# Kernel tuning notes

Measured on AMD Instinct MI355X. Metric: run time of the kernel, lower is better.

Reference implementation:

```python
import jax, jax.numpy as jnp
import numpy as np

# --- dims ---
B_, H_IMG, W_IMG = 8, 64, 1024
C1, C2 = 32, 64
DM = 1024          # token channels = C2 * H_IMG/4
DI = 2048          # d_inner = expand * d_model
DS = 64            # d_state
DC = 4             # d_conv
NH, HD = 32, 64    # n_heads, headdim
DCONV_DIM = DI + 2 * DS           # 2176 (ngroups=1)
DPROJ = 2 * DI + 2 * DS + NH      # 4256
NB = 4             # num mamba blocks
FFH = 2 * DM       # feed-forward hidden
EPS = 1e-5


def bn(x, p, axis=1):
    # eval-mode batchnorm; p = [gamma, beta, running_mean, running_var] stacked [4, C]
    sh = [1] * x.ndim
    sh[axis] = -1
    g, b, m, v = (p[i].reshape(sh) for i in range(4))
    return (x - m) * jax.lax.rsqrt(v + EPS) * g + b


def conv2d(x, w, stride, pad):
    return jax.lax.conv_general_dilated(
        x, w, (stride, stride), [(pad, pad), (pad, pad)],
        dimension_numbers=("NCHW", "OIHW", "NCHW"))


def mamba2(u, Wi, cw, cb, dtb, A_log, Dp, nw, Wo):
    # u: [B, L, DM]  (faithful Mamba2 forward: in_proj -> causal depthwise conv
    #  + silu -> selective state scan -> gated RMSNorm -> out_proj)
    Bsz, L, _ = u.shape
    zxbcdt = jnp.einsum('bld,pd->blp', u, Wi)                  # [B,L,DPROJ]
    z, xBC, dt = jnp.split(zxbcdt, [DI, DI + DCONV_DIM], axis=-1)
    dt = jax.nn.softplus(dt + dtb)                             # [B,L,NH]
    xp = jnp.pad(xBC, ((0, 0), (DC - 1, 0), (0, 0)))           # causal pad
    xBC = sum(xp[:, k:k + L, :] * cw[:, k] for k in range(DC)) + cb
    xBC = jax.nn.silu(xBC)
    x, Bm, Cm = jnp.split(xBC, [DI, DI + DS], axis=-1)         # x:[B,L,DI] B/C:[B,L,DS]
    x = x.reshape(Bsz, L, NH, HD)
    A = -jnp.exp(A_log)                                        # [NH]
    dA = jnp.exp(dt * A)                                       # [B,L,NH]
    dtx = dt[..., None] * x                                    # [B,L,NH,HD]

    def step(h, inp):
        dA_t, dtx_t, B_t, C_t = inp
        h = h * dA_t[..., None, None] + dtx_t[..., None] * B_t[:, None, None, :]
        return h, jnp.einsum('bhpn,bn->bhp', h, C_t)

    h0 = jnp.zeros((Bsz, NH, HD, DS), u.dtype)
    _, ys = jax.lax.scan(step, h0, (dA.transpose(1, 0, 2),
                                    dtx.transpose(1, 0, 2, 3),
                                    Bm.transpose(1, 0, 2),
                                    Cm.transpose(1, 0, 2)))
    y = ys.transpose(1, 0, 2, 3) + Dp[None, None, :, None] * x  # D skip
    y = y.reshape(Bsz, L, DI)
    y = y * jax.nn.silu(z)                                      # gate
    y = y * jax.lax.rsqrt(jnp.mean(y * y, -1, keepdims=True) + EPS) * nw
    return jnp.einsum('bld,od->blo', y, Wo)                     # [B,L,DM]


def setup_inputs() -> dict:
    key = jax.random.key(0)
    ks = iter(jax.random.split(key, 80))

    def nrm(shape, s=0.02):
        return jax.random.normal(next(ks), shape, jnp.float32) * s

    def bnp(c):
        return jnp.stack([jax.random.uniform(next(ks), (c,), minval=0.5, maxval=1.5),
                          nrm((c,), 0.1), nrm((c,), 0.1),
                          jax.random.uniform(next(ks), (c,), minval=0.5, maxval=1.5)])

    inp = dict(
        image=jax.random.normal(next(ks), (B_, 1, H_IMG, W_IMG), jnp.float32),
        conv1_w=nrm((C1, 1, 7, 7), 0.1), bn1=bnp(C1),
        conv2_w=nrm((C2, C1, 7, 7), 0.05), bn2=bnp(C2),
        ds_w=nrm((C2, 1, 1, 1), 0.1), ds_bn=bnp(C2),
        in_proj_w=nrm((NB, DPROJ, DM)),
        conv1d_w=nrm((NB, DCONV_DIM, DC), 0.2), conv1d_b=nrm((NB, DCONV_DIM), 0.1),
        dt_bias=jnp.log(jnp.expm1(jax.random.uniform(next(ks), (NB, NH), minval=0.001, maxval=0.1))),
        A_log=jnp.log(jax.random.uniform(next(ks), (NB, NH), minval=1.0, maxval=16.0)),
        D=jax.random.uniform(next(ks), (NB, NH)),
        norm_w=jnp.ones((NB, DI), jnp.float32),
        out_proj_w=nrm((NB, DM, DI)),
        blk_bn=jnp.stack([bnp(DM) for _ in range(NB)]),
        ff_w1=nrm((NB, FFH, DM)), ff_b1=nrm((NB, FFH), 0.1),
        ff_bn1=jnp.stack([bnp(FFH) for _ in range(NB)]),
        ff_w2=nrm((NB, DM, FFH)), ff_b2=nrm((NB, DM), 0.1),
        ff_bn2=jnp.stack([bnp(DM) for _ in range(NB)]),
    )
    return inp


def reference(image, conv1_w, bn1, conv2_w, bn2, ds_w, ds_bn,
              in_proj_w, conv1d_w, conv1d_b, dt_bias, A_log, D, norm_w,
              out_proj_w, blk_bn, ff_w1, ff_b1, ff_bn1, ff_w2, ff_b2, ff_bn2):
    # --- conv stem with residual downsample ---
    x = bn(conv2d(image, conv1_w, 2, 3), bn1)
    x = bn(conv2d(x, conv2_w, 2, 3), bn2)
    res = bn(conv2d(image, ds_w, 4, 0), ds_bn)
    x = jax.nn.relu(x + res)                       # [B,C2,H/4,W/4]
    tokens = x.reshape(x.shape[0], -1, x.shape[3])  # image_to_sequence -> [B,DM,L]

    for i in range(NB):
        # SSMBlock: mamba2 + BN + residual
        residual = tokens
        t = mamba2(tokens.transpose(0, 2, 1), in_proj_w[i], conv1d_w[i],
                   conv1d_b[i], dt_bias[i], A_log[i], D[i], norm_w[i],
                   out_proj_w[i]).transpose(0, 2, 1)
        tokens = bn(t, blk_bn[i]) + residual
        # FeedForward (1x1 conv MLP) with residual
        residual = tokens
        h = jax.nn.relu(bn(jnp.einsum('oc,bcl->bol', ff_w1[i], tokens)
                           + ff_b1[i][:, None], ff_bn1[i]))
        tokens = bn(jnp.einsum('oc,bcl->bol', ff_w2[i], h)
                    + ff_b2[i][:, None], ff_bn2[i]) + residual
    return tokens  # [B, DM, L]
```

## Files before the change

kernel.cpp:

```cpp
#include <hip/hip_runtime.h>
#include <hip/hip_bf16.h>
#include <hip/hip_fp16.h>
#include <math.h>

#define EPSF 1e-5f
#define B_N 8
#define L_N 256
#define DM_N 1024
#define DI_N 2048
#define DS_N 64
#define NH_N 32
#define HD_N 64
#define DCONV_N 2176
#define DPROJ_N 4256
#define NTOK 2048
#define FFH_N 2048
#define NPAD_INPROJ 4352

typedef _Float16 f16x8 __attribute__((ext_vector_type(8)));
typedef float f32x4 __attribute__((ext_vector_type(4)));

__device__ __forceinline__ float sigf(float x) { return 1.f / (1.f + __expf(-x)); }

__device__ __forceinline__ void gll16(const void* g, void* l) {
  typedef __attribute__((address_space(1))) const void gv;
  typedef __attribute__((address_space(3))) void lv;
  __builtin_amdgcn_global_load_lds((gv*)g, (lv*)l, 16, 0, 0);
}

__device__ __forceinline__ f16x8 cvt8(float4 a, float4 b) {
  f16x8 o;
  o[0] = (_Float16)a.x; o[1] = (_Float16)a.y; o[2] = (_Float16)a.z; o[3] = (_Float16)a.w;
  o[4] = (_Float16)b.x; o[5] = (_Float16)b.y; o[6] = (_Float16)b.z; o[7] = (_Float16)b.w;
  return o;
}

__global__ __launch_bounds__(256) void k_tohalf8(
    const float* __restrict__ src, _Float16* __restrict__ dst, int n, int ntot) {
  int i = (blockIdx.x * 256 + threadIdx.x) * 8;
  if (i >= ntot) return;
  f16x8 o;
  if (i < n) {
    float4 a = *(const float4*)(src + i);
    float4 b = *(const float4*)(src + i + 4);
    o = cvt8(a, b);
  } else {
#pragma unroll
    for (int j = 0; j < 8; ++j) o[j] = (_Float16)0.f;
  }
  *(f16x8*)(dst + i) = o;
}

__global__ __launch_bounds__(256) void k_w1t(
    const float* __restrict__ w1, _Float16* __restrict__ W1t) {
  int i = blockIdx.x * 256 + threadIdx.x;
  if (i >= 32 * 64) return;
  int co = i >> 6, k = i & 63;
  W1t[i] = (k < 49) ? (_Float16)w1[co * 49 + k] : (_Float16)0.f;
}

__global__ __launch_bounds__(256) void k_conv1m(
    const float* __restrict__ img, const _Float16* __restrict__ W1t,
    const float* __restrict__ bnp, _Float16* __restrict__ X1h) {
  __shared__ float sIn[7][264];
  __shared__ _Float16 sA[128][72];
  __shared__ _Float16 sB[32][72];
  int b = blockIdx.x, y = blockIdx.y, x0 = blockIdx.z * 128;
  int t = threadIdx.x;
  {
    int r = t >> 3, c = (t & 7) * 8;
    *(f16x8*)&sB[r][c] = *(const f16x8*)&W1t[r * 64 + c];
  }
  const float* ip = img + (size_t)b * 64 * 1024;
#pragma unroll
  for (int r = 0; r < 7; ++r) {
    int yy = 2 * y - 3 + r;
    for (int c = t; c < 262; c += 256) {
      int xx = 2 * x0 - 3 + c;
      float v = 0.f;
      if (yy >= 0 && yy < 64 && xx >= 0 && xx < 1024) v = ip[yy * 1024 + xx];
      sIn[r][c] = v;
    }
  }
  __syncthreads();
  {
    int p = t >> 1, half = t & 1;
    _Float16 av[32];
    if (half == 0) {
#pragma unroll
      for (int k = 0; k < 32; ++k)
        av[k] = (_Float16)sIn[k / 7][2 * p + (k % 7)];
    } else {
#pragma unroll
      for (int k = 32; k < 64; ++k)
        av[k - 32] = (k < 49) ? (_Float16)sIn[k / 7][2 * p + (k % 7)] : (_Float16)0.f;
    }
    *(f16x8*)&sA[p][half * 32 + 0] = *(f16x8*)&av[0];
    *(f16x8*)&sA[p][half * 32 + 8] = *(f16x8*)&av[8];
    *(f16x8*)&sA[p][half * 32 + 16] = *(f16x8*)&av[16];
    *(f16x8*)&sA[p][half * 32 + 24] = *(f16x8*)&av[24];
  }
  __syncthreads();
  int w = t >> 6, lane = t & 63, lr = lane & 15, kh = lane >> 4;
  f32x4 acc[2][2];
#pragma unroll
  for (int i = 0; i < 2; ++i)
#pragma unroll
    for (int j = 0; j < 2; ++j) acc[i][j] = (f32x4)(0.f);
#pragma unroll
  for (int ks = 0; ks < 2; ++ks) {
    f16x8 af[2], bf[2];
#pragma unroll
    for (int i = 0; i < 2; ++i)
      af[i] = *(const f16x8*)&sA[w * 32 + i * 16 + lr][ks * 32 + kh * 8];
#pragma unroll
    for (int j = 0; j < 2; ++j)
      bf[j] = *(const f16x8*)&sB[j * 16 + lr][ks * 32 + kh * 8];
#pragma unroll
    for (int i = 0; i < 2; ++i)
#pragma unroll
      for (int j = 0; j < 2; ++j)
        acc[i][j] = __builtin_amdgcn_mfma_f32_16x16x32_f16(af[i], bf[j], acc[i][j], 0, 0, 0);
  }
#pragma unroll
  for (int j = 0; j < 2; ++j) {
    int co = j * 16 + lr;
    float g = bnp[co], be = bnp[32 + co], mm = bnp[64 + co], vv = bnp[96 + co];
    float sc = rsqrtf(vv + EPSF) * g, sh = be - mm * sc;
#pragma unroll
    for (int i = 0; i < 2; ++i) {
#pragma unroll
      for (int rr = 0; rr < 4; ++rr) {
        int pix = w * 32 + i * 16 + kh * 4 + rr;
        int x = x0 + pix;
        X1h[((size_t)(b * 32 + y) * 512 + x) * 32 + co] =
            (_Float16)fmaf(acc[i][j][rr], sc, sh);
      }
    }
  }
}

__global__ __launch_bounds__(256) void k_w2t(
    const float* __restrict__ w2, _Float16* __restrict__ W2t) {
  int i = blockIdx.x * 256 + threadIdx.x;
  if (i >= 49 * 64 * 32) return;
  int ci = i & 31, co = (i >> 5) & 63, rs = i >> 11;
  W2t[rs * 2048 + co * 32 + ci] = (_Float16)w2[co * 1568 + ci * 49 + rs];
}

__global__ __launch_bounds__(512) void k_conv2m(
    const _Float16* __restrict__ X1h, const _Float16* __restrict__ W2t,
    const float* __restrict__ bn2p, const float* __restrict__ img,
    const float* __restrict__ dsw, const float* __restrict__ dsbnp,
    _Float16* __restrict__ Tok16) {
  __shared__ _Float16 As[2][128 * 40];
  __shared__ _Float16 Bs[2][64 * 40];
  int b = blockIdx.x, ho = blockIdx.y, wo0 = blockIdx.z * 128;
  int t = threadIdx.x;
  int w = t >> 6, lane = t & 63;
  int lr = lane & 15, kh = lane >> 4;
  int wm = w >> 1, wn = w & 1;
  f32x4 acc[2][2];
#pragma unroll
  for (int i = 0; i < 2; ++i)
#pragma unroll
    for (int j = 0; j < 2; ++j) acc[i][j] = (f32x4)(0.f);

  int arow = t >> 2, achk = t & 3;
  const _Float16* xb = X1h + (size_t)b * 32 * 512 * 32;

  auto LOADA = [&](int rs, f16x8& ra) {
    int r = rs / 7, s = rs - 7 * r;
    int y = 2 * ho + r - 3;
    int xx = 2 * (wo0 + arow) + s - 3;
    if (y >= 0 && y < 32 && xx >= 0 && xx < 512)
      ra = *(const f16x8*)(xb + ((size_t)(y * 512 + xx)) * 32 + achk * 8);
    else
      ra = (f16x8)(_Float16)0.f;
  };

  f16x8 ra, rb;
  LOADA(0, ra);
  if (t < 256) rb = *(const f16x8*)(W2t + (t >> 2) * 32 + (t & 3) * 8);
  *(f16x8*)&As[0][arow * 40 + achk * 8] = ra;
  if (t < 256) *(f16x8*)&Bs[0][(t >> 2) * 40 + (t & 3) * 8] = rb;
  __syncthreads();

  int cur = 0;
  for (int rs = 0; rs < 49; ++rs) {
    f16x8 na, nb;
    if (rs + 1 < 49) {
      LOADA(rs + 1, na);
      if (t < 256)
        nb = *(const f16x8*)(W2t + (rs + 1) * 2048 + (t >> 2) * 32 + (t & 3) * 8);
    }
    f16x8 af[2], bf[2];
#pragma unroll
    for (int i = 0; i < 2; ++i)
      af[i] = *(const f16x8*)&As[cur][(wm * 32 + i * 16 + lr) * 40 + kh * 8];
#pragma unroll
    for (int j = 0; j < 2; ++j)
      bf[j] = *(const f16x8*)&Bs[cur][(wn * 32 + j * 16 + lr) * 40 + kh * 8];
#pragma unroll
    for (int i = 0; i < 2; ++i)
#pragma unroll
      for (int j = 0; j < 2; ++j)
        acc[i][j] = __builtin_amdgcn_mfma_f32_16x16x32_f16(af[i], bf[j], acc[i][j], 0, 0, 0);
    if (rs + 1 < 49) {
      *(f16x8*)&As[cur ^ 1][arow * 40 + achk * 8] = na;
      if (t < 256) *(f16x8*)&Bs[cur ^ 1][(t >> 2) * 40 + (t & 3) * 8] = nb;
      __syncthreads();
      cur ^= 1;
    }
  }

#pragma unroll
  for (int j = 0; j < 2; ++j) {
    int co = wn * 32 + j * 16 + lr;
    float g = bn2p[co], be = bn2p[64 + co], mm = bn2p[128 + co], vv = bn2p[192 + co];
    float sc = rsqrtf(vv + EPSF) * g, sh = be - mm * sc;
    float dg = dsbnp[co], dbe = dsbnp[64 + co], dmm = dsbnp[128 + co], dvv = dsbnp[192 + co];
    float dsc = rsqrtf(dvv + EPSF) * dg, dsh = dbe - dmm * dsc;
    float wv = dsw[co];
#pragma unroll
    for (int i = 0; i < 2; ++i) {
#pragma unroll
      for (int rr = 0; rr < 4; ++rr) {
        int row = wm * 32 + i * 16 + kh * 4 + rr;
        int wo = wo0 + row;
        float dval = fmaf(img[((size_t)(b * 64 + 4 * ho)) * 1024 + 4 * wo] * wv, dsc, dsh);
        float v = fmaf(acc[i][j][rr], sc, sh) + dval;
        v = v > 0.f ? v : 0.f;
        Tok16[((size_t)(b * 256 + wo)) * DM_N + co * 16 + ho] = (_Float16)v;
      }
    }
  }
}

template <int MODE, int BM, int BN>
__global__ __launch_bounds__(256) void k_mgemm(
    const _Float16* __restrict__ A, const _Float16* __restrict__ W,
    int M, int N, int K,
    const float* __restrict__ bias, const float* __restrict__ bnp,
    const _Float16* __restrict__ res16, _Float16* __restrict__ C16) {
  constexpr int MI = BM / 32, NJ = BN / 32;
  __shared__ _Float16 As[2][BM * 32];
  __shared__ _Float16 Bs[2][BN * 32];
  const int t = threadIdx.x;
  const int w = t >> 6, lane = t & 63;
  const int lr = lane & 15, kh = lane >> 4;
  const int wm = w >> 1, wn = w & 1;
  const int m0 = blockIdx.y * BM, n0 = blockIdx.x * BN;
  f32x4 acc[MI][NJ];
#pragma unroll
  for (int i = 0; i < MI; ++i)
#pragma unroll
    for (int j = 0; j < NJ; ++j) acc[i][j] = (f32x4)(0.f);

  const int nt = K >> 5;
  auto STAGE = [&](int bb, int kt) {
    const int k0 = kt << 5;
#pragma unroll
    for (int it = 0; it < BM / 64; ++it) {
      int c = it * 256 + w * 64 + lane;
      int row = c >> 2, kq = c & 3;
      gll16(A + (size_t)(m0 + row) * K + k0 + kq * 8,
            &As[bb][(size_t)(it * 256 + w * 64) * 8]);
    }
#pragma unroll
    for (int it = 0; it < BN / 64; ++it) {
      int c = it * 256 + w * 64 + lane;
      int row = c >> 2, kq = c & 3;
      gll16(W + (size_t)(n0 + row) * K + k0 + kq * 8,
            &Bs[bb][(size_t)(it * 256 + w * 64) * 8]);
    }
  };

  STAGE(0, 0);
  __syncthreads();
  int bb = 0;
  for (int kt = 0; kt < nt; ++kt) {
    if (kt + 1 < nt) STAGE(bb ^ 1, kt + 1);
    f16x8 af[MI], bf[NJ];
#pragma unroll
    for (int i = 0; i < MI; ++i)
      af[i] = *(const f16x8*)&As[bb][(size_t)((wm * (BM / 2) + i * 16 + lr) * 32 + kh * 8)];
#pragma unroll
    for (int j = 0; j < NJ; ++j)
      bf[j] = *(const f16x8*)&Bs[bb][(size_t)((wn * (BN / 2) + j * 16 + lr) * 32 + kh * 8)];
#pragma unroll
    for (int i = 0; i < MI; ++i)
#pragma unroll
      for (int j = 0; j < NJ; ++j)
        acc[i][j] = __builtin_amdgcn_mfma_f32_16x16x32_f16(af[i], bf[j], acc[i][j], 0, 0, 0);
    __syncthreads();
    bb ^= 1;
  }

#pragma unroll
  for (int j = 0; j < NJ; ++j) {
    int cn = n0 + wn * (BN / 2) + j * 16 + lr;
    if (cn >= N) continue;
    float sc = 1.f, sh = 0.f, bs = 0.f;
    if (MODE >= 1) {
      float g = bnp[cn], be = bnp[N + cn];
      float mm = bnp[2 * N + cn], vv = bnp[3 * N + cn];
      sc = rsqrtf(vv + EPSF) * g;
      sh = be - mm * sc;
    }
    if (MODE == 2 || MODE == 3) bs = bias[cn];
#pragma unroll
    for (int i = 0; i < MI; ++i) {
#pragma unroll
      for (int rr = 0; rr < 4; ++rr) {
        int r = m0 + wm * (BM / 2) + i * 16 + kh * 4 + rr;
        float v = acc[i][j][rr];
        if (MODE == 2 || MODE == 3) v += bs;
        if (MODE >= 1) v = fmaf(v, sc, sh);
        if (MODE == 2) v = v > 0.f ? v : 0.f;
        size_t o = (size_t)r * N + cn;
        if (MODE == 1 || MODE == 3) v += (float)res16[o];
        C16[o] = (_Float16)v;
      }
    }
  }
}

__global__ __launch_bounds__(256) void k_convprep(
    const _Float16* __restrict__ ZX16, const float* __restrict__ cw,
    const float* __restrict__ cb, const float* __restrict__ dtb,
    const float* __restrict__ Alog, _Float16* __restrict__ XBC16,
    float* __restrict__ DT, float* __restrict__ DLA) {
  int m = blockIdx.x;
  int c = blockIdx.y * 256 + threadIdx.x;
  int l = m & 255;
  if (c < DCONV_N) {
    const float* cwp = cw + c * 4;
    float acc = cb[c];
#pragma unroll
    for (int k = 0; k < 4; ++k) {
      int dl = l + k - 3;
      if (dl >= 0)
        acc = fmaf((float)ZX16[(size_t)(m + k - 3) * DPROJ_N + DI_N + c], cwp[k], acc);
    }
    XBC16[(size_t)m * DCONV_N + c] = (_Float16)(acc * sigf(acc));
  } else if (c < DCONV_N + NH_N) {
    int h = c - DCONV_N;
    float xx = (float)ZX16[(size_t)m * DPROJ_N + DI_N + DCONV_N + h] + dtb[h];
    float dt = xx > 20.f ? xx : log1pf(__expf(xx));
    DT[m * NH_N + h] = dt;
    DLA[m * NH_N + h] = -dt * __expf(Alog[h]);
  }
}

__global__ __launch_bounds__(256) void k_scan(
    const _Float16* __restrict__ XBC16, const float* __restrict__ DT,
    const float* __restrict__ DLA, const float* __restrict__ Dp,
    float* __restrict__ Y) {
  __shared__ _Float16 sC[64][72];
  __shared__ _Float16 sB[64][72];
  __shared__ _Float16 sBts[64][72];
  __shared__ _Float16 sXt[64][72];
  __shared__ _Float16 sP[64][72];
  __shared__ _Float16 sH[64][72];
  __shared__ float sH32[64][68];
  __shared__ float sS[64], sEl[64], sEs[64], sDt[64];
  __shared__ float sCpt;

  const int b = blockIdx.x >> 5, h = blockIdx.x & 31;
  const int t = threadIdx.x;
  const int w = t >> 6, lane = t & 63;
  const int lr = lane & 15, kh = lane >> 4;
  const float Dh = Dp[h];

  {
    _Float16* hp = &sH[0][0];
    float* h32p = &sH32[0][0];
    for (int i = t; i < 64 * 72; i += 256) hp[i] = (_Float16)0.f;
    for (int i = t; i < 64 * 68; i += 256) h32p[i] = 0.f;
  }

  for (int c = 0; c < 4; ++c) {
    const int mbase = b * L_N + c * 64;
    __syncthreads();

    if (t < 64) {
      int l = t;
      float v = DLA[(mbase + l) * NH_N + h];
#pragma unroll
      for (int o = 1; o < 64; o <<= 1) {
        float u = __shfl_up(v, o);
        v += (l >= o) ? u : 0.f;
      }
      sS[l] = v;
      sEl[l] = __expf(v);
      float s63 = __shfl(v, 63);
      sEs[l] = __expf(s63 - v);
      if (l == 63) sCpt = __expf(s63);
      sDt[l] = DT[(mbase + l) * NH_N + h];
    }
    __syncthreads();

    {
      int l = t >> 2, q = t & 3;
      const _Float16* row = XBC16 + (size_t)(mbase + l) * DCONV_N;
      float dt_l = sDt[l], es_l = sEs[l];
      f16x8 b0 = *(const f16x8*)&row[DI_N + q * 16];
      f16x8 b1 = *(const f16x8*)&row[DI_N + q * 16 + 8];
      *(f16x8*)&sB[l][q * 16] = b0;
      *(f16x8*)&sB[l][q * 16 + 8] = b1;
#pragma unroll
      for (int i = 0; i < 8; ++i) {
        sBts[q * 16 + i][l] = (_Float16)((float)b0[i] * es_l);
        sBts[q * 16 + 8 + i][l] = (_Float16)((float)b1[i] * es_l);
      }
      *(f16x8*)&sC[l][q * 16] = *(const f16x8*)&row[DI_N + DS_N + q * 16];
      *(f16x8*)&sC[l][q * 16 + 8] = *(const f16x8*)&row[DI_N + DS_N + q * 16 + 8];
      f16x8 x0 = *(const f16x8*)&row[h * HD_N + q * 16];
      f16x8 x1 = *(const f16x8*)&row[h * HD_N + q * 16 + 8];
#pragma unroll
      for (int i = 0; i < 8; ++i) {
        sXt[q * 16 + i][l] = (_Float16)((float)x0[i] * dt_l);
        sXt[q * 16 + 8 + i][l] = (_Float16)((float)x1[i] * dt_l);
      }
    }
    __syncthreads();

    f32x4 Sacc[4], Yacc[4];
#pragma unroll
    for (int j = 0; j < 4; ++j) { Sacc[j] = (f32x4)(0.f); Yacc[j] = (f32x4)(0.f); }
    {
      f16x8 aC[2];
#pragma unroll
      for (int kk = 0; kk < 2; ++kk)
        aC[kk] = *(const f16x8*)&sC[16 * w + lr][kk * 32 + kh * 8];
#pragma unroll
      for (int kk = 0; kk < 2; ++kk)
#pragma unroll
        for (int jt = 0; jt < 4; ++jt) {
          f16x8 bB = *(const f16x8*)&sB[jt * 16 + lr][kk * 32 + kh * 8];
          f16x8 bH = *(const f16x8*)&sH[jt * 16 + lr][kk * 32 + kh * 8];
          Sacc[jt] = __builtin_amdgcn_mfma_f32_16x16x32_f16(aC[kk], bB, Sacc[jt], 0, 0, 0);
          Yacc[jt] = __builtin_amdgcn_mfma_f32_16x16x32_f16(aC[kk], bH, Yacc[jt], 0, 0, 0);
        }
    }

#pragma unroll
    for (int rr = 0; rr < 4; ++rr) {
      int l = 16 * w + kh * 4 + rr;
      float sl = sS[l], el = sEl[l];
#pragma unroll
      for (int jt = 0; jt < 4; ++jt) {
        int j = jt * 16 + lr;
        float pv = (j <= l) ? Sacc[jt][rr] * __expf(sl - sS[j]) : 0.f;
        sP[l][j] = (_Float16)pv;
        Yacc[jt][rr] *= el;
      }
    }
    __syncthreads();

    f32x4 Hacc[4];
#pragma unroll
    for (int j = 0; j < 4; ++j) Hacc[j] = (f32x4)(0.f);
    {
      f16x8 aP[2], aX[2];
#pragma unroll
      for (int kk = 0; kk < 2; ++kk) {
        aP[kk] = *(const f16x8*)&sP[16 * w + lr][kk * 32 + kh * 8];
        aX[kk] = *(const f16x8*)&sXt[16 * w + lr][kk * 32 + kh * 8];
      }
#pragma unroll
      for (int kk = 0; kk < 2; ++kk)
#pragma unroll
        for (int jt = 0; jt < 4; ++jt) {
          f16x8 bX = *(const f16x8*)&sXt[jt * 16 + lr][kk * 32 + kh * 8];
          f16x8 bBt = *(const f16x8*)&sBts[jt * 16 + lr][kk * 32 + kh * 8];
          Yacc[jt] = __builtin_amdgcn_mfma_f32_16x16x32_f16(aP[kk], bX, Yacc[jt], 0, 0, 0);
          Hacc[jt] = __builtin_amdgcn_mfma_f32_16x16x32_f16(aX[kk], bBt, Hacc[jt], 0, 0, 0);
        }
    }

    float cpt = sCpt;
#pragma unroll
    for (int rr = 0; rr < 4; ++rr) {
      int lrow = 16 * w + kh * 4 + rr;
      int m = mbase + lrow;
#pragma unroll
      for (int jt = 0; jt < 4; ++jt) {
        int p = jt * 16 + lr;
        float xr = (float)XBC16[(size_t)m * DCONV_N + h * HD_N + p];
        Y[(size_t)m * DI_N + h * HD_N + p] = fmaf(Dh, xr, Yacc[jt][rr]);
        float hv = fmaf(cpt, sH32[lrow][jt * 16 + lr], Hacc[jt][rr]);
        sH32[lrow][jt * 16 + lr] = hv;
        sH[lrow][jt * 16 + lr] = (_Float16)hv;
      }
    }
  }
}

__global__ __launch_bounds__(256) void k_gatenorm(
    const float* __restrict__ Y, const _Float16* __restrict__ ZX16,
    const float* __restrict__ nw, _Float16* __restrict__ YN16) {
  int m = blockIdx.x, t = threadIdx.x;
  const float* y = Y + (size_t)m * DI_N;
  const _Float16* z = ZX16 + (size_t)m * DPROJ_N;
  int c0 = t * 8;
  float4 y0 = *(const float4*)&y[c0];
  float4 y1 = *(const float4*)&y[c0 + 4];
  f16x8 z8 = *(const f16x8*)&z[c0];
  float yv[8] = {y0.x, y0.y, y0.z, y0.w, y1.x, y1.y, y1.z, y1.w};
  float vals[8];
  float ss = 0.f;
#pragma unroll
  for (int j = 0; j < 8; ++j) {
    float zz = (float)z8[j];
    float vv = yv[j] * zz * sigf(zz);
    vals[j] = vv;
    ss = fmaf(vv, vv, ss);
  }
#pragma unroll
  for (int o = 1; o < 64; o <<= 1) ss += __shfl_xor(ss, o);
  __shared__ float sred[4];
  if ((t & 63) == 0) sred[t >> 6] = ss;
  __syncthreads();
  float tot = sred[0] + sred[1] + sred[2] + sred[3];
  float scale = rsqrtf(tot * (1.f / DI_N) + EPSF);
  float4 nw0 = *(const float4*)&nw[c0];
  float4 nw1 = *(const float4*)&nw[c0 + 4];
  float nv[8] = {nw0.x, nw0.y, nw0.z, nw0.w, nw1.x, nw1.y, nw1.z, nw1.w};
  f16x8 o;
#pragma unroll
  for (int j = 0; j < 8; ++j) o[j] = (_Float16)(vals[j] * scale * nv[j]);
  *(f16x8*)&YN16[(size_t)m * DI_N + c0] = o;
}

__global__ __launch_bounds__(256) void k_transpose(
    const _Float16* __restrict__ Tok16, float* __restrict__ out) {
  __shared__ float tile[32][33];
  int d0 = blockIdx.x * 32, m0 = blockIdx.y * 32;
  int tx = threadIdx.x & 31, ty = threadIdx.x >> 5;
  for (int i = ty; i < 32; i += 8)
    tile[i][tx] = (float)Tok16[(size_t)(m0 + i) * DM_N + d0 + tx];
  __syncthreads();
  int b = m0 >> 8, l0 = m0 & 255;
  for (int i = ty; i < 32; i += 8)
    out[((size_t)b * DM_N + d0 + i) * L_N + l0 + tx] = tile[tx][i];
}

extern "C" void kernel_launch(void* const* d_in, const int* in_sizes, int n_in,
                              void* d_out, int out_size, void* d_ws, size_t ws_size,
                              hipStream_t stream) {
  const float* image = (const float*)d_in[0];
  const float* conv1_w = (const float*)d_in[1];
  const float* bn1 = (const float*)d_in[2];
  const float* conv2_w = (const float*)d_in[3];
  const float* bn2 = (const float*)d_in[4];
  const float* ds_w = (const float*)d_in[5];
  const float* ds_bn = (const float*)d_in[6];
  const float* in_proj_w = (const float*)d_in[7];
  const float* conv1d_w = (const float*)d_in[8];
  const float* conv1d_b = (const float*)d_in[9];
  const float* dt_bias = (const float*)d_in[10];
  const float* A_log = (const float*)d_in[11];
  const float* Dpar = (const float*)d_in[12];
  const float* norm_w = (const float*)d_in[13];
  const float* out_proj_w = (const float*)d_in[14];
  const float* blk_bn = (const float*)d_in[15];
  const float* ff_w1 = (const float*)d_in[16];
  const float* ff_b1 = (const float*)d_in[17];
  const float* ff_bn1 = (const float*)d_in[18];
  const float* ff_w2 = (const float*)d_in[19];
  const float* ff_b2 = (const float*)d_in[20];
  const float* ff_bn2 = (const float*)d_in[21];

  float* ws = (float*)d_ws;
  float* YR = ws;
  float* DTb = YR + (size_t)NTOK * DI_N;
  float* DLAb = DTb + (size_t)NTOK * NH_N;
  _Float16* Tok16 = (_Float16*)(DLAb + (size_t)NTOK * NH_N);
  _Float16* ZX16 = Tok16 + (size_t)NTOK * DM_N;
  _Float16* XBC16 = ZX16 + (size_t)NTOK * DPROJ_N;
  _Float16* YN16 = XBC16 + (size_t)NTOK * DCONV_N;
  _Float16* H116 = YN16 + (size_t)NTOK * DI_N;
  _Float16* W16 = H116 + (size_t)NTOK * DI_N;
  _Float16* W2t = W16 + (size_t)NPAD_INPROJ * DM_N;
  _Float16* W1t = W2t + (size_t)49 * 64 * 32;
  _Float16* X1h = (_Float16*)YR;

  k_w1t<<<8, 256, 0, stream>>>(conv1_w, W1t);
  k_conv1m<<<dim3(8, 32, 4), 256, 0, stream>>>(image, W1t, bn1, X1h);
  k_w2t<<<(49 * 64 * 32 + 255) / 256, 256, 0, stream>>>(conv2_w, W2t);
  k_conv2m<<<dim3(8, 16, 2), 512, 0, stream>>>(X1h, W2t, bn2, image, ds_w, ds_bn, Tok16);

  for (int i = 0; i < 4; ++i) {
    const float* Wi = in_proj_w + (size_t)i * DPROJ_N * DM_N;
    const float* cw = conv1d_w + (size_t)i * DCONV_N * 4;
    const float* cb = conv1d_b + (size_t)i * DCONV_N;
    const float* dtb = dt_bias + i * NH_N;
    const float* al = A_log + i * NH_N;
    const float* dd = Dpar + i * NH_N;
    const float* nw = norm_w + i * DI_N;
    const float* Wo = out_proj_w + (size_t)i * DM_N * DI_N;
    const float* bbn = blk_bn + (size_t)i * 4 * DM_N;
    const float* w1 = ff_w1 + (size_t)i * FFH_N * DM_N;
    const float* b1 = ff_b1 + i * FFH_N;
    const float* fbn1 = ff_bn1 + (size_t)i * 4 * FFH_N;
    const float* w2 = ff_w2 + (size_t)i * DM_N * FFH_N;
    const float* b2 = ff_b2 + i * DM_N;
    const float* fbn2 = ff_bn2 + (size_t)i * 4 * DM_N;

    k_tohalf8<<<(NPAD_INPROJ * 1024 / 8 + 255) / 256, 256, 0, stream>>>(
        Wi, W16, DPROJ_N * DM_N, NPAD_INPROJ * DM_N);
    k_mgemm<0, 64, 128><<<dim3(34, 32), 256, 0, stream>>>(
        Tok16, W16, NTOK, DPROJ_N, DM_N, nullptr, nullptr, nullptr, ZX16);
    k_convprep<<<dim3(NTOK, 9), 256, 0, stream>>>(ZX16, cw, cb, dtb, al, XBC16, DTb, DLAb);
    k_scan<<<256, 256, 0, stream>>>(XBC16, DTb, DLAb, dd, YR);
    k_gatenorm<<<NTOK, 256, 0, stream>>>(YR, ZX16, nw, YN16);
    k_tohalf8<<<(DM_N * DI_N / 8 + 255) / 256, 256, 0, stream>>>(
        Wo, W16, DM_N * DI_N, DM_N * DI_N);
    k_mgemm<1, 64, 64><<<dim3(16, 32), 256, 0, stream>>>(
        YN16, W16, NTOK, DM_N, DI_N, nullptr, bbn, Tok16, Tok16);
    k_tohalf8<<<(FFH_N * DM_N / 8 + 255) / 256, 256, 0, stream>>>(
        w1, W16, FFH_N * DM_N, FFH_N * DM_N);
    k_mgemm<2, 64, 128><<<dim3(16, 32), 256, 0, stream>>>(
        Tok16, W16, NTOK, FFH_N, DM_N, b1, fbn1, nullptr, H116);
    k_tohalf8<<<(DM_N * FFH_N / 8 + 255) / 256, 256, 0, stream>>>(
        w2, W16, DM_N * FFH_N, DM_N * FFH_N);
    k_mgemm<3, 64, 64><<<dim3(16, 32), 256, 0, stream>>>(
        H116, W16, NTOK, DM_N, FFH_N, b2, fbn2, Tok16, Tok16);
  }
  k_transpose<<<dim3(32, 64), 256, 0, stream>>>(Tok16, (float*)d_out);
}
```

Before: 754.1 us.

## Double K-step per stage in MFMA GEMM with XOR-swizzled LDS and retile conv2

The generic MFMA GEMM now stages 64-wide K tiles instead of 32, which halves the number of barriers per K loop. It applies an XOR swizzle on the 16-byte chunk index so LDS reads avoid bank conflicts without padding. The conv2 implicit GEMM is retiled to 64-pixel blocks of 256 threads that consume two filter taps per stage, with a padded LDS stride of 72. In exchange, LDS use per block doubles, which may reduce occupancy, and conv2 does a padded 50th tap.

```diff
diff --git a/kernel.cpp b/kernel.cpp
--- a/kernel.cpp
+++ b/kernel.cpp
@@ -148,14 +148,14 @@
   W2t[rs * 2048 + co * 32 + ci] = (_Float16)w2[co * 1568 + ci * 49 + rs];
 }
 
-__global__ __launch_bounds__(512) void k_conv2m(
+__global__ __launch_bounds__(256) void k_conv2m(
     const _Float16* __restrict__ X1h, const _Float16* __restrict__ W2t,
     const float* __restrict__ bn2p, const float* __restrict__ img,
     const float* __restrict__ dsw, const float* __restrict__ dsbnp,
     _Float16* __restrict__ Tok16) {
-  __shared__ _Float16 As[2][128 * 40];
-  __shared__ _Float16 Bs[2][64 * 40];
-  int b = blockIdx.x, ho = blockIdx.y, wo0 = blockIdx.z * 128;
+  __shared__ _Float16 As[2][64 * 72];
+  __shared__ _Float16 Bs[2][64 * 72];
+  int b = blockIdx.x, ho = blockIdx.y, wo0 = blockIdx.z * 64;
   int t = threadIdx.x;
   int w = t >> 6, lane = t & 63;
   int lr = lane & 15, kh = lane >> 4;
@@ -166,49 +166,75 @@
 #pragma unroll
     for (int j = 0; j < 2; ++j) acc[i][j] = (f32x4)(0.f);
 
-  int arow = t >> 2, achk = t & 3;
   const _Float16* xb = X1h + (size_t)b * 32 * 512 * 32;
 
-  auto LOADA = [&](int rs, f16x8& ra) {
-    int r = rs / 7, s = rs - 7 * r;
-    int y = 2 * ho + r - 3;
-    int xx = 2 * (wo0 + arow) + s - 3;
-    if (y >= 0 && y < 32 && xx >= 0 && xx < 512)
-      ra = *(const f16x8*)(xb + ((size_t)(y * 512 + xx)) * 32 + achk * 8);
-    else
-      ra = (f16x8)(_Float16)0.f;
+  auto LOADA = [&](int step, int u, f16x8& ra) {
+    int c = u * 256 + t;
+    int row = c >> 3, s = c & 7;
+    int rsl = s >> 2, ciq = s & 3;
+    int rs = step * 2 + rsl;
+#pragma unroll
+    for (int q = 0; q < 8; ++q) ra[q] = (_Float16)0.f;
+    if (rs < 49) {
+      int r = rs / 7, ss = rs - 7 * r;
+      int y = 2 * ho + r - 3, xx = 2 * (wo0 + row) + ss - 3;
+      if (y >= 0 && y < 32 && xx >= 0 && xx < 512)
+        ra = *(const f16x8*)(xb + ((size_t)(y * 512 + xx)) * 32 + ciq * 8);
+    }
   };
-
-  f16x8 ra, rb;
-  LOADA(0, ra);
-  if (t < 256) rb = *(const f16x8*)(W2t + (t >> 2) * 32 + (t & 3) * 8);
-  *(f16x8*)&As[0][arow * 40 + achk * 8] = ra;
-  if (t < 256) *(f16x8*)&Bs[0][(t >> 2) * 40 + (t & 3) * 8] = rb;
+  auto LOADB = [&](int step, int u, f16x8& rb) {
+    int c = u * 256 + t;
+    int co = c >> 3, s = c & 7;
+    int rsl = s >> 2, ciq = s & 3;
+    int rs = step * 2 + rsl;
+#pragma unroll
+    for (int q = 0; q < 8; ++q) rb[q] = (_Float16)0.f;
+    if (rs < 49) rb = *(const f16x8*)(W2t + rs * 2048 + co * 32 + ciq * 8);
+  };
+
+  f16x8 ra[2], rb[2];
+#pragma unroll
+  for (int u = 0; u < 2; ++u) { LOADA(0, u, ra[u]); LOADB(0, u, rb[u]); }
+#pragma unroll
+  for (int u = 0; u < 2; ++u) {
+    int c = u * 256 + t, row = c >> 3, s = c & 7;
+    *(f16x8*)&As[0][row * 72 + s * 8] = ra[u];
+    *(f16x8*)&Bs[0][row * 72 + s * 8] = rb[u];
+  }
   __syncthreads();
 
   int cur = 0;
-  for (int rs = 0; rs < 49; ++rs) {
-    f16x8 na, nb;
-    if (rs + 1 < 49) {
-      LOADA(rs + 1, na);
-      if (t < 256)
-        nb = *(const f16x8*)(W2t + (rs + 1) * 2048 + (t >> 2) * 32 + (t & 3) * 8);
-    }
-    f16x8 af[2], bf[2];
+  for (int st = 0; st < 25; ++st) {
+    f16x8 na[2], nb[2];
+    if (st + 1 < 25) {
+#pragma unroll
+      for (int u = 0; u < 2; ++u) { LOADA(st + 1, u, na[u]); LOADB(st + 1, u, nb[u]); }
+    }
+    f16x8 af[2][2], bf[2][2];
 #pragma unroll
     for (int i = 0; i < 2; ++i)
-      af[i] = *(const f16x8*)&As[cur][(wm * 32 + i * 16 + lr) * 40 + kh * 8];
+#pragma unroll
+      for (int kk = 0; kk < 2; ++kk)
+        af[i][kk] = *(const f16x8*)&As[cur][(wm * 32 + i * 16 + lr) * 72 + (kk * 4 + kh) * 8];
 #pragma unroll
     for (int j = 0; j < 2; ++j)
-      bf[j] = *(const f16x8*)&Bs[cur][(wn * 32 + j * 16 + lr) * 40 + kh * 8];
-#pragma unroll
-    for (int i = 0; i < 2; ++i)
-#pragma unroll
-      for (int j = 0; j < 2; ++j)
-        acc[i][j] = __builtin_amdgcn_mfma_f32_16x16x32_f16(af[i], bf[j], acc[i][j], 0, 0, 0);
-    if (rs + 1 < 49) {
-      *(f16x8*)&As[cur ^ 1][arow * 40 + achk * 8] = na;
-      if (t < 256) *(f16x8*)&Bs[cur ^ 1][(t >> 2) * 40 + (t & 3) * 8] = nb;
+#pragma unroll
+      for (int kk = 0; kk < 2; ++kk)
+        bf[j][kk] = *(const f16x8*)&Bs[cur][(wn * 32 + j * 16 + lr) * 72 + (kk * 4 + kh) * 8];
+#pragma unroll
+    for (int kk = 0; kk < 2; ++kk)
+#pragma unroll
+      for (int i = 0; i < 2; ++i)
+#pragma unroll
+        for (int j = 0; j < 2; ++j)
+          acc[i][j] = __builtin_amdgcn_mfma_f32_16x16x32_f16(af[i][kk], bf[j][kk], acc[i][j], 0, 0, 0);
+    if (st + 1 < 25) {
+#pragma unroll
+      for (int u = 0; u < 2; ++u) {
+        int c = u * 256 + t, row = c >> 3, s = c & 7;
+        *(f16x8*)&As[cur ^ 1][row * 72 + s * 8] = na[u];
+        *(f16x8*)&Bs[cur ^ 1][row * 72 + s * 8] = nb[u];
+      }
       __syncthreads();
       cur ^= 1;
     }
@@ -244,8 +270,8 @@
     const float* __restrict__ bias, const float* __restrict__ bnp,
     const _Float16* __restrict__ res16, _Float16* __restrict__ C16) {
   constexpr int MI = BM / 32, NJ = BN / 32;
-  __shared__ _Float16 As[2][BM * 32];
-  __shared__ _Float16 Bs[2][BN * 32];
+  __shared__ _Float16 As[2][BM * 64];
+  __shared__ _Float16 Bs[2][BN * 64];
   const int t = threadIdx.x;
   const int w = t >> 6, lane = t & 63;
   const int lr = lane & 15, kh = lane >> 4;
@@ -257,21 +283,23 @@
 #pragma unroll
     for (int j = 0; j < NJ; ++j) acc[i][j] = (f32x4)(0.f);
 
-  const int nt = K >> 5;
+  const int nt = K >> 6;
   auto STAGE = [&](int bb, int kt) {
-    const int k0 = kt << 5;
-#pragma unroll
-    for (int it = 0; it < BM / 64; ++it) {
+    const int k0 = kt << 6;
+#pragma unroll
+    for (int it = 0; it < BM / 32; ++it) {
       int c = it * 256 + w * 64 + lane;
-      int row = c >> 2, kq = c & 3;
-      gll16(A + (size_t)(m0 + row) * K + k0 + kq * 8,
+      int row = c >> 3, s = c & 7;
+      int kg = (s ^ (row & 7)) * 8;
+      gll16(A + (size_t)(m0 + row) * K + k0 + kg,
             &As[bb][(size_t)(it * 256 + w * 64) * 8]);
     }
 #pragma unroll
-    for (int it = 0; it < BN / 64; ++it) {
+    for (int it = 0; it < BN / 32; ++it) {
       int c = it * 256 + w * 64 + lane;
-      int row = c >> 2, kq = c & 3;
-      gll16(W + (size_t)(n0 + row) * K + k0 + kq * 8,
+      int row = c >> 3, s = c & 7;
+      int kg = (s ^ (row & 7)) * 8;
+      gll16(W + (size_t)(n0 + row) * K + k0 + kg,
             &Bs[bb][(size_t)(it * 256 + w * 64) * 8]);
     }
   };
@@ -279,20 +307,29 @@
   STAGE(0, 0);
   __syncthreads();
   int bb = 0;
+  const int sw = lr & 7;
   for (int kt = 0; kt < nt; ++kt) {
     if (kt + 1 < nt) STAGE(bb ^ 1, kt + 1);
-    f16x8 af[MI], bf[NJ];
+    f16x8 af[MI][2], bf[NJ][2];
 #pragma unroll
     for (int i = 0; i < MI; ++i)
-      af[i] = *(const f16x8*)&As[bb][(size_t)((wm * (BM / 2) + i * 16 + lr) * 32 + kh * 8)];
+#pragma unroll
+      for (int kk = 0; kk < 2; ++kk)
+        af[i][kk] = *(const f16x8*)&As[bb][(size_t)(wm * (BM / 2) + i * 16 + lr) * 64 +
+                                           ((kk * 4 + kh) ^ sw) * 8];
 #pragma unroll
     for (int j = 0; j < NJ; ++j)
-      bf[j] = *(const f16x8*)&Bs[bb][(size_t)((wn * (BN / 2) + j * 16 + lr) * 32 + kh * 8)];
-#pragma unroll
-    for (int i = 0; i < MI; ++i)
-#pragma unroll
-      for (int j = 0; j < NJ; ++j)
-        acc[i][j] = __builtin_amdgcn_mfma_f32_16x16x32_f16(af[i], bf[j], acc[i][j], 0, 0, 0);
+#pragma unroll
+      for (int kk = 0; kk < 2; ++kk)
+        bf[j][kk] = *(const f16x8*)&Bs[bb][(size_t)(wn * (BN / 2) + j * 16 + lr) * 64 +
+                                           ((kk * 4 + kh) ^ sw) * 8];
+#pragma unroll
+    for (int kk = 0; kk < 2; ++kk)
+#pragma unroll
+      for (int i = 0; i < MI; ++i)
+#pragma unroll
+        for (int j = 0; j < NJ; ++j)
+          acc[i][j] = __builtin_amdgcn_mfma_f32_16x16x32_f16(af[i][kk], bf[j][kk], acc[i][j], 0, 0, 0);
     __syncthreads();
     bb ^= 1;
   }
@@ -590,7 +627,7 @@
   k_w1t<<<8, 256, 0, stream>>>(conv1_w, W1t);
   k_conv1m<<<dim3(8, 32, 4), 256, 0, stream>>>(image, W1t, bn1, X1h);
   k_w2t<<<(49 * 64 * 32 + 255) / 256, 256, 0, stream>>>(conv2_w, W2t);
-  k_conv2m<<<dim3(8, 16, 2), 512, 0, stream>>>(X1h, W2t, bn2, image, ds_w, ds_bn, Tok16);
+  k_conv2m<<<dim3(8, 16, 4), 256, 0, stream>>>(X1h, W2t, bn2, image, ds_w, ds_bn, Tok16);
 
   for (int i = 0; i < 4; ++i) {
     const float* Wi = in_proj_w + (size_t)i * DPROJ_N * DM_N;
```

New measurement: 691.4 us. 8.3% less time.
